# Optimization experiments

Measured on AMD Instinct MI355X. Metric: run time of the kernel, lower is better.

## Reference

```python
import jax, jax.numpy as jnp
import numpy as np

C = 512
B, W, H = 16, 64, 64
K = 128


def setup_inputs() -> dict:
    key = jax.random.key(0)
    ks = jax.random.split(key, 17)
    s = 0.02
    inp = {
        "x1": jax.random.normal(ks[0], (B, C, W, H), jnp.float32),
        "y1": jax.random.normal(ks[1], (B, K, C), jnp.float32),
        "x2": jax.random.normal(ks[2], (B, C, W, H), jnp.float32),
        "y2": jax.random.normal(ks[3], (B, K, C), jnp.float32),
        # 1x1 conv weights stored as [out, in]
        "wq1": jax.random.normal(ks[4], (C // 4, C), jnp.float32) * s,
        "bq1": jnp.zeros((C // 4,), jnp.float32),
        "wq2": jax.random.normal(ks[5], (C // 4, C), jnp.float32) * s,
        "bq2": jnp.zeros((C // 4,), jnp.float32),
        "wk1": jax.random.normal(ks[6], (C // 2, C), jnp.float32) * s,
        "bk1": jnp.zeros((C // 2,), jnp.float32),
        "wk2": jax.random.normal(ks[7], (C // 2, C), jnp.float32) * s,
        "bk2": jnp.zeros((C // 2,), jnp.float32),
        "wv1": jax.random.normal(ks[8], (C, C), jnp.float32) * s,
        "bv1": jnp.zeros((C,), jnp.float32),
        "wv2": jax.random.normal(ks[9], (C, C), jnp.float32) * s,
        "bv2": jnp.zeros((C,), jnp.float32),
        "scale": jnp.ones((1,), jnp.float32) * 0.5,  # nn.Parameter(zeros) would kill grads; nonzero for testing
    }
    return inp


def reference(x1, y1, x2, y2, wq1, bq1, wq2, bq2, wk1, bk1, wk2, bk2,
              wv1, bv1, wv2, bv2, scale):
    b, c, w, h = x1.shape
    n = w * h
    # 1x1 convs == channel-wise linear maps
    q1 = jnp.einsum('bcwh,dc->bdwh', x1, wq1) + bq1[None, :, None, None]
    q2 = jnp.einsum('bcwh,dc->bdwh', x2, wq2) + bq2[None, :, None, None]
    # concat along channels -> [B, C/2, N] -> [B, N, C/2]
    q = jnp.concatenate([q1, q2], axis=1).reshape(b, c // 2, n).transpose(0, 2, 1)
    k1 = y1 @ wk1.T + bk1  # [B, K, C/2]
    k2 = y2 @ wk2.T + bk2
    v1 = y1 @ wv1.T + bv1  # [B, K, C]
    v2 = y2 @ wv2.T + bv2
    e1 = jnp.einsum('bnd,bkd->bnk', q, k1)  # [B, N, K]
    e2 = jnp.einsum('bnd,bkd->bnk', q, k2)
    attn = jax.nn.softmax(jnp.abs(e1 - e2), axis=-1)
    # out = value^T @ attn^T : [B, C, N]
    o1 = jnp.einsum('bkc,bnk->bcn', v1, attn).reshape(b, c, w, h)
    o2 = jnp.einsum('bkc,bnk->bcn', v2, attn).reshape(b, c, w, h)
    out1 = scale[0] * o1 + x1
    out2 = scale[0] * o2 + x2
    return out1, out2
```

## Files before the change

### kernel.cpp

```cpp
#include <hip/hip_runtime.h>

typedef unsigned short u16;
typedef __attribute__((ext_vector_type(8))) short short8v;
typedef __attribute__((ext_vector_type(4))) unsigned short ushort4v;
typedef __attribute__((ext_vector_type(4))) float floatx4;

#define B_ 16
#define C_ 512
#define N_ 4096
#define K_ 128

__device__ __forceinline__ float bf2f(u16 u) {
    unsigned int x = ((unsigned int)u) << 16;
    return __builtin_bit_cast(float, x);
}
__device__ __forceinline__ u16 f2bf(float f) {
    unsigned int u = __builtin_bit_cast(unsigned int, f);
    u = u + 0x7FFFu + ((u >> 16) & 1u);
    return (u16)(u >> 16);
}
__device__ __forceinline__ void gload_lds16(const u16* g, u16* l) {
    __builtin_amdgcn_global_load_lds(
        (const __attribute__((address_space(1))) void*)g,
        (__attribute__((address_space(3))) void*)l, 16, 0, 0);
}

#define BARRIER_V8 do { \
    asm volatile("s_waitcnt vmcnt(8) lgkmcnt(0)" ::: "memory"); \
    __builtin_amdgcn_s_barrier(); \
    __builtin_amdgcn_sched_barrier(0); \
} while (0)
#define BARRIER_V0 do { \
    asm volatile("s_waitcnt vmcnt(0) lgkmcnt(0)" ::: "memory"); \
    __builtin_amdgcn_s_barrier(); \
    __builtin_amdgcn_sched_barrier(0); \
} while (0)

__global__ void conv_all(const float* __restrict__ y1, const float* __restrict__ y2,
                         const float* __restrict__ wk1, const float* __restrict__ wk2,
                         const float* __restrict__ wv1, const float* __restrict__ wv2,
                         const float* __restrict__ wq1, const float* __restrict__ wq2,
                         u16* y1b, u16* y2b, u16* wk1b, u16* wk2b, u16* wv1b, u16* wv2b,
                         u16* wq1t, u16* wq2t) {
    int tid = blockIdx.x * 256 + threadIdx.x;
    const int VBASE = 720896;
    if (tid < VBASE) {
        const float* src; u16* dst; int off;
        if (tid < 262144)      { src = y1;  dst = y1b;  off = tid; }
        else if (tid < 524288) { src = y2;  dst = y2b;  off = tid - 262144; }
        else if (tid < 557056) { src = wk1; dst = wk1b; off = tid - 524288; }
        else if (tid < 589824) { src = wk2; dst = wk2b; off = tid - 557056; }
        else if (tid < 655360) { src = wv1; dst = wv1b; off = tid - 589824; }
        else                   { src = wv2; dst = wv2b; off = tid - 655360; }
        float4 v = *(const float4*)(src + (size_t)off * 4);
        ushort4v p;
        p[0] = f2bf(v.x); p[1] = f2bf(v.y); p[2] = f2bf(v.z); p[3] = f2bf(v.w);
        *(ushort4v*)(dst + (size_t)off * 4) = p;
    } else {
        int e = tid - VBASE;
        const float* s = (e >= 65536) ? wq2 : wq1;
        u16* d = (e >= 65536) ? wq2t : wq1t;
        e &= 65535;
        int dd = e >> 9;
        int c = e & 511;
        d[c * 128 + dd] = f2bf(s[dd * 512 + c]);
    }
}

__global__ void gemm_gkgv(const u16* __restrict__ y1b, const u16* __restrict__ y2b,
// ... 78 lines not shown
        int koff = ch * 32 + (l >> 4) * 8;
        short8v a[4], wv[4];
#pragma unroll
        for (int mf = 0; mf < 4; ++mf) {
            size_t ro = (size_t)(m0 + mf*16 + (l & 15)) * 256 + koff;
            short8v s1 = *(const short8v*)(A1 + ro);
            short8v s2 = *(const short8v*)(A2 + ro);
            short8v av;
#pragma unroll
            for (int j = 0; j < 8; ++j)
                av[j] = (short)f2bf(bf2f((u16)s1[j]) - bf2f((u16)s2[j]));
            a[mf] = av;
        }
#pragma unroll
        for (int nf = 0; nf < 4; ++nf) wv[nf] = *(const short8v*)(Wt + (size_t)(n0 + nf*16 + (l & 15)) * 128 + koff);
#pragma unroll
        for (int mf = 0; mf < 4; ++mf)
#pragma unroll
            for (int nf = 0; nf < 4; ++nf)
                acc[mf][nf] = __builtin_amdgcn_mfma_f32_16x16x32_bf16(a[mf], wv[nf], acc[mf][nf], 0, 0, 0);
    }
#pragma unroll
    for (int mf = 0; mf < 4; ++mf)
#pragma unroll
        for (int nf = 0; nf < 4; ++nf)
#pragma unroll
            for (int rg = 0; rg < 4; ++rg) {
                int m = m0 + mf*16 + (l >> 4)*4 + rg;
                int n = n0 + nf*16 + (l & 15);
                outp[(size_t)m * C_ + n] = f2bf(acc[mf][nf][rg]);
            }
}

__global__ __launch_bounds__(256, 2)
void fused_attn(const float* __restrict__ x1, const float* __restrict__ x2,
                const u16* __restrict__ kkd1, const u16* __restrict__ kkd2,
                const u16* __restrict__ vt1, const u16* __restrict__ vt2,
                const float* __restrict__ ebd, const float* __restrict__ scale_p,
                float* __restrict__ out1, float* __restrict__ out2) {
    __shared__ u16 smem[32768];
    u16* xT[2]  = { smem,         smem + 8192 };
    u16* kkS[2] = { smem + 16384, smem + 24576 };
    u16* attn_s = smem + 16384;

    int id = blockIdx.x;
    int sw = ((id & 7) << 6) | (id >> 3);
    int b = sw >> 5;
    int n0 = (sw & 31) * 128;
    int t = threadIdx.x, w = t >> 6, l = t & 63;

    const float* xs[2] = { x1 + (size_t)b * C_ * N_, x2 + (size_t)b * C_ * N_ };
    const u16* kkp[2] = { kkd1 + (size_t)b * K_ * C_, kkd2 + (size_t)b * K_ * C_ };

    floatx4 ed[2][8] = {};

    float xA0[16], xA1[16], xB0[16], xB1[16];

    auto SLOADX = [&](int s, float (&v0)[16], float (&v1)[16]) {
        int h = s >> 3, c0 = (s & 7) * 64;
        const float* xp = xs[h] + (size_t)(c0 + w * 16) * N_ + n0 + 2 * l;
#pragma unroll
        for (int j = 0; j < 16; ++j) {
            float2 f = *(const float2*)(xp + (size_t)j * N_);
            v0[j] = f.x; v1[j] = f.y;
        }
    };
    auto KLDS = [&](int s, int buf) {
        int h = s >> 3, c0 = (s & 7) * 64;
        const u16* kp = kkp[h] + c0;
#pragma unroll
        for (int i = 0; i < 4; ++i) {
            int gi = i * 256 + t;
            int key = gi >> 3, gp = gi & 7;
            gload_lds16(kp + (size_t)key * 512 + (gp ^ (key & 7)) * 8,
                        &kkS[buf][(i * 256 + w * 64) * 8]);
        }
    };
    auto SWRITEX = [&](int buf, float (&v0)[16], float (&v1)[16]) {
        short8v p00, p01, p10, p11;
#pragma unroll
        for (int j = 0; j < 8; ++j) {
            p00[j] = (short)f2bf(v0[j]);  p01[j] = (short)f2bf(v0[j + 8]);
            p10[j] = (short)f2bf(v1[j]);  p11[j] = (short)f2bf(v1[j + 8]);
        }
        u16* xb = xT[buf];
        int row0 = 2 * l, sz = l & 7;
        *(short8v*)&xb[row0 * 64 + 8 * ((w * 2) ^ sz)] = p00;
        *(short8v*)&xb[row0 * 64 + 8 * ((w * 2 + 1) ^ sz)] = p01;
        *(short8v*)&xb[(row0 + 1) * 64 + 8 * ((w * 2) ^ sz)] = p10;
        *(short8v*)&xb[(row0 + 1) * 64 + 8 * ((w * 2 + 1) ^ sz)] = p11;
    };
    auto COMPUTE = [&](int buf) {
        u16* xb = xT[buf]; u16* kb = kkS[buf];
#pragma unroll
        for (int cc = 0; cc < 2; ++cc) {
            short8v a[2];
#pragma unroll
            for (int mf = 0; mf < 2; ++mf) {
                int row = w * 32 + mf * 16 + (l & 15);
                int g = cc * 4 + (l >> 4);
                a[mf] = *(const short8v*)&xb[row * 64 + 8 * (g ^ ((row >> 1) & 7))];
            }
#pragma unroll
            for (int kf = 0; kf < 8; ++kf) {
                int key = kf * 16 + (l & 15);
                int g = cc * 4 + (l >> 4);
                short8v bb = *(const short8v*)&kb[key * 64 + 8 * (g ^ (key & 7))];
#pragma unroll
                for (int mf = 0; mf < 2; ++mf)
                    ed[mf][kf] = __builtin_amdgcn_mfma_f32_16x16x32_bf16(a[mf], bb, ed[mf][kf], 0, 0, 0);
            }
        }
    };

    SLOADX(0, xA0, xA1); KLDS(0, 0);
    SWRITEX(0, xA0, xA1);
    SLOADX(1, xB0, xB1); KLDS(1, 1);
#pragma unroll
    for (int rr = 0; rr < 8; ++rr) {
        int sA = 2 * rr, sB = 2 * rr + 1;
        BARRIER_V8;
        if (rr > 0) KLDS(sB, 1);
        COMPUTE(0);
        SWRITEX(1, xB0, xB1);
        if (sA + 2 <= 15) SLOADX(sA + 2, xA0, xA1);
        if (rr == 7) { BARRIER_V0; }
        else         { BARRIER_V8; }
        if (sA + 2 <= 15) KLDS(sA + 2, 0);
        COMPUTE(1);
        if (sB + 1 <= 15) SWRITEX(0, xA0, xA1);
        if (sB + 2 <= 15) SLOADX(sB + 2, xB0, xB1);
    }

    float ebv[8];
#pragma unroll
    for (int kf = 0; kf < 8; ++kf) ebv[kf] = ebd[b * 128 + kf * 16 + (l & 15)];
#pragma unroll
    for (int mf = 0; mf < 2; ++mf)
#pragma unroll
        for (int kf = 0; kf < 8; ++kf)
#pragma unroll
            for (int rg = 0; rg < 4; ++rg)
                ed[mf][kf][rg] = fabsf(ed[mf][kf][rg] + ebv[kf]);

    float mx[2][4], sm[2][4];
#pragma unroll
    for (int mf = 0; mf < 2; ++mf)
#pragma unroll
        for (int rg = 0; rg < 4; ++rg) {
            float m = fmaxf(ed[mf][0][rg], ed[mf][1][rg]);
            m = fmaxf(m, fmaxf(ed[mf][2][rg], ed[mf][3][rg]));
            m = fmaxf(m, fmaxf(ed[mf][4][rg], ed[mf][5][rg]));
            m = fmaxf(m, fmaxf(ed[mf][6][rg], ed[mf][7][rg]));
            mx[mf][rg] = m;
        }
#pragma unroll
    for (int st = 1; st < 16; st <<= 1)
#pragma unroll
        for (int mf = 0; mf < 2; ++mf)
#pragma unroll
            for (int rg = 0; rg < 4; ++rg)
                mx[mf][rg] = fmaxf(mx[mf][rg], __shfl_xor(mx[mf][rg], st));
#pragma unroll
    for (int mf = 0; mf < 2; ++mf)
#pragma unroll
        for (int rg = 0; rg < 4; ++rg) sm[mf][rg] = 0.f;
#pragma unroll
    for (int mf = 0; mf < 2; ++mf)
#pragma unroll
        for (int kf = 0; kf < 8; ++kf)
#pragma unroll
            for (int rg = 0; rg < 4; ++rg) {
                float e = __expf(ed[mf][kf][rg] - mx[mf][rg]);
                ed[mf][kf][rg] = e;
                sm[mf][rg] += e;
            }
#pragma unroll
    for (int st = 1; st < 16; st <<= 1)
#pragma unroll
        for (int mf = 0; mf < 2; ++mf)
#pragma unroll
            for (int rg = 0; rg < 4; ++rg)
                sm[mf][rg] += __shfl_xor(sm[mf][rg], st);
#pragma unroll
    for (int mf = 0; mf < 2; ++mf)
#pragma unroll
        for (int rg = 0; rg < 4; ++rg) sm[mf][rg] = 1.0f / sm[mf][rg];

    __syncthreads();
#pragma unroll
    for (int mf = 0; mf < 2; ++mf)
#pragma unroll
        for (int rg = 0; rg < 4; ++rg) {
            int row = w * 32 + mf * 16 + (l >> 4) * 4 + rg;
#pragma unroll
            for (int kf = 0; kf < 8; ++kf) {
                int col = kf * 16 + (l & 15);
                attn_s[row * 128 + 8 * ((col >> 3) ^ (row & 15)) + (col & 7)] =
                    f2bf(ed[mf][kf][rg] * sm[mf][rg]);
            }
        }
    __syncthreads();

    const float sc = scale_p[0];
    const u16* vts[2] = { vt1 + (size_t)b * C_ * K_, vt2 + (size_t)b * C_ * K_ };
    float* outs[2] = { out1 + (size_t)b * C_ * N_, out2 + (size_t)b * C_ * N_ };

    short8v vfA[4], vfB[4];
    float rsA[4][8], rsB[4][8];
    auto LOADPV = [&](int s, short8v (&vf)[4], float (&rs)[4][8]) {
        int oi = s >> 3, cc = s & 7;
        const u16* vp = vts[oi] + (size_t)(cc * 64 + w * 16 + (l & 15)) * K_ + (l >> 4) * 8;
#pragma unroll
        for (int kc = 0; kc < 4; ++kc) vf[kc] = *(const short8v*)(vp + kc * 32);
        const float* rp = xs[oi] + (size_t)(cc * 64 + w * 16 + (l >> 4) * 4) * N_ + n0 + (l & 15);
#pragma unroll
        for (int rg = 0; rg < 4; ++rg)
#pragma unroll
            for (int nf = 0; nf < 8; ++nf)
                rs[rg][nf] = rp[(size_t)rg * N_ + nf * 16];
    };
    auto COMPPV = [&](int s, short8v (&vf)[4], float (&rs)[4][8]) {
        floatx4 o[8] = {};
#pragma unroll
        for (int kc = 0; kc < 4; ++kc) {
#pragma unroll
            for (int nf = 0; nf < 8; ++nf) {
                int row = nf * 16 + (l & 15);
                int g = kc * 4 + (l >> 4);
                short8v bb = *(const short8v*)&attn_s[row * 128 + 8 * (g ^ (row & 15))];
                o[nf] = __builtin_amdgcn_mfma_f32_16x16x32_bf16(vf[kc], bb, o[nf], 0, 0, 0);
            }
        }
        int oi = s >> 3, cc = s & 7;
        float* op = outs[oi];
        int cr = cc * 64 + w * 16 + (l >> 4) * 4;
#pragma unroll
        for (int rg = 0; rg < 4; ++rg) {
            size_t rowoff = (size_t)(cr + rg) * N_ + n0 + (l & 15);
#pragma unroll
            for (int nf = 0; nf < 8; ++nf)
                op[rowoff + nf * 16] = sc * o[nf][rg] + rs[rg][nf];
        }
    };

    LOADPV(0, vfA, rsA);
    LOADPV(1, vfB, rsB);
#pragma unroll
    for (int ss = 0; ss < 8; ++ss) {
        COMPPV(2 * ss, vfA, rsA);
        if (2 * ss + 2 < 16) LOADPV(2 * ss + 2, vfA, rsA);
        COMPPV(2 * ss + 1, vfB, rsB);
        if (2 * ss + 3 < 16) LOADPV(2 * ss + 3, vfB, rsB);
    }
}

extern "C" void kernel_launch(void* const* d_in, const int* in_sizes, int n_in,
                              void* d_out, int out_size, void* d_ws, size_t ws_size,
                              hipStream_t stream) {
    const float* x1 = (const float*)d_in[0];
    const float* y1 = (const float*)d_in[1];
    const float* x2 = (const float*)d_in[2];
    const float* y2 = (const float*)d_in[3];
    const float* wq1 = (const float*)d_in[4];
    const float* bq1 = (const float*)d_in[5];
    const float* wq2 = (const float*)d_in[6];
    const float* bq2 = (const float*)d_in[7];
    const float* wk1 = (const float*)d_in[8];
    const float* bk1 = (const float*)d_in[9];
    const float* wk2 = (const float*)d_in[10];
    const float* bk2 = (const float*)d_in[11];
    const float* wv1 = (const float*)d_in[12];
    const float* bv1 = (const float*)d_in[13];
    const float* wv2 = (const float*)d_in[14];
    const float* bv2 = (const float*)d_in[15];
    const float* scale = (const float*)d_in[16];

    char* ws = (char*)d_ws;
    u16* y1b  = (u16*)(ws + 0);
    u16* y2b  = (u16*)(ws + 2097152);
    u16* wk1b = (u16*)(ws + 4194304);
    u16* wk2b = (u16*)(ws + 4456448);
    u16* wv1b = (u16*)(ws + 4718592);
    u16* wv2b = (u16*)(ws + 5242880);
    u16* wq1t = (u16*)(ws + 5767168);
    u16* wq2t = (u16*)(ws + 5898240);
    u16* k1b  = (u16*)(ws + 6029312);
    u16* k2b  = (u16*)(ws + 7077888);
    u16* kkd1 = (u16*)(ws + 9175040);
    u16* kkd2 = (u16*)(ws + 11272192);
    u16* vt1  = (u16*)(ws + 13369344);
    u16* vt2  = (u16*)(ws + 15466496);
    float* ebd = (float*)(ws + 17563648);

    float* out1 = (float*)d_out;
    float* out2 = out1 + (size_t)B_ * C_ * N_;

    hipLaunchKernelGGL(conv_all, dim3(3328), dim3(256), 0, stream,
                       y1, y2, wk1, wk2, wv1, wv2, wq1, wq2,
                       y1b, y2b, wk1b, wk2b, wv1b, wv2b, wq1t, wq2t);
    hipLaunchKernelGGL(gemm_gkgv, dim3(768), dim3(64), 0, stream,
                       y1b, y2b, wk1b, wk2b, wv1b, wv2b, bk1, bk2, bv1, bv2,
                       k1b, k2b, vt1, vt2);
    hipLaunchKernelGGL(gemm_gkk_ebd, dim3(544), dim3(64), 0, stream,
                       k1b, k2b, wq1t, wq2t, bq1, bq2, kkd1, kkd2, ebd);
    hipLaunchKernelGGL(fused_attn, dim3(512), dim3(256), 0, stream,
                       x1, x2, kkd1, kkd2, vt1, vt2, ebd, scale, out1, out2);
}
```

Before: 213.2 us.

## Process two N-tiles per block, overlapping second QK pass with first PV pass

Each block of the fused attention kernel now handles two 128-column tiles, so the grid is halved to 256 blocks. While the PV output pass of the first tile runs, the QK score accumulation of the second tile proceeds in the same loop, interleaving MFMA work with the x/K loads. LDS grows to hold a separate attention buffer, and the softmax becomes a macro that runs once per tile. The risks are fewer blocks to fill the CUs (256 blocks of 256 threads), higher register pressure, and extra barriers in the merged loop.

After: 315.2 us. +47.8%, slower.

```diff
diff --git a/kernel.cpp b/kernel.cpp
--- a/kernel.cpp
+++ b/kernel.cpp
@@ -185,34 +185,43 @@
                 const u16* __restrict__ vt1, const u16* __restrict__ vt2,
                 const float* __restrict__ ebd, const float* __restrict__ scale_p,
                 float* __restrict__ out1, float* __restrict__ out2) {
-    __shared__ u16 smem[32768];
-    u16* xT[2]  = { smem,         smem + 8192 };
-    u16* kkS[2] = { smem + 16384, smem + 24576 };
-    u16* attn_s = smem + 16384;
+    __shared__ u16 smem[40960];
+    u16* xTb[2] = { smem, smem + 8192 };
+    u16* kkS0   = smem + 16384;
+    u16* attn_s = smem + 24576;
+    u16* attnlo = smem + 24576;
 
     int id = blockIdx.x;
-    int sw = ((id & 7) << 6) | (id >> 3);
-    int b = sw >> 5;
-    int n0 = (sw & 31) * 128;
+    int sw = ((id & 7) << 5) | (id >> 3);
+    int b  = sw >> 4;
+    int n0 = (sw & 15) * 256;
+    int n1 = n0 + 128;
     int t = threadIdx.x, w = t >> 6, l = t & 63;
 
     const float* xs[2] = { x1 + (size_t)b * C_ * N_, x2 + (size_t)b * C_ * N_ };
     const u16* kkp[2] = { kkd1 + (size_t)b * K_ * C_, kkd2 + (size_t)b * K_ * C_ };
+    const u16* vts[2] = { vt1 + (size_t)b * C_ * K_, vt2 + (size_t)b * C_ * K_ };
+    float* outs[2] = { out1 + (size_t)b * C_ * N_, out2 + (size_t)b * C_ * N_ };
+    const float sc = scale_p[0];
 
     floatx4 ed[2][8] = {};
+    float ebv[8];
+#pragma unroll
+    for (int kf = 0; kf < 8; ++kf) ebv[kf] = ebd[b * 128 + kf * 16 + (l & 15)];
 
     float xA0[16], xA1[16], xB0[16], xB1[16];
-
-    auto SLOADX = [&](int s, float (&v0)[16], float (&v1)[16]) {
+    short8v vfA[4], vfB[4];
+
+    auto SLOADX = [&](int n, int s, float (&v0)[16], float (&v1)[16]) {
         int h = s >> 3, c0 = (s & 7) * 64;
-        const float* xp = xs[h] + (size_t)(c0 + w * 16) * N_ + n0 + 2 * l;
+        const float* xp = xs[h] + (size_t)(c0 + w * 16) * N_ + n + 2 * l;
 #pragma unroll
         for (int j = 0; j < 16; ++j) {
             float2 f = *(const float2*)(xp + (size_t)j * N_);
             v0[j] = f.x; v1[j] = f.y;
         }
     };
-    auto KLDS = [&](int s, int buf) {
+    auto KLDS = [&](int s, u16* kb) {
         int h = s >> 3, c0 = (s & 7) * 64;
         const u16* kp = kkp[h] + c0;
 #pragma unroll
@@ -220,7 +229,7 @@
             int gi = i * 256 + t;
             int key = gi >> 3, gp = gi & 7;
             gload_lds16(kp + (size_t)key * 512 + (gp ^ (key & 7)) * 8,
-                        &kkS[buf][(i * 256 + w * 64) * 8]);
+                        &kb[(i * 256 + w * 64) * 8]);
         }
     };
     auto SWRITEX = [&](int buf, float (&v0)[16], float (&v1)[16]) {
@@ -230,15 +239,14 @@
             p00[j] = (short)f2bf(v0[j]);  p01[j] = (short)f2bf(v0[j + 8]);
             p10[j] = (short)f2bf(v1[j]);  p11[j] = (short)f2bf(v1[j + 8]);
         }
-        u16* xb = xT[buf];
+        u16* xb = xTb[buf];
         int row0 = 2 * l, sz = l & 7;
         *(short8v*)&xb[row0 * 64 + 8 * ((w * 2) ^ sz)] = p00;
         *(short8v*)&xb[row0 * 64 + 8 * ((w * 2 + 1) ^ sz)] = p01;
         *(short8v*)&xb[(row0 + 1) * 64 + 8 * ((w * 2) ^ sz)] = p10;
         *(short8v*)&xb[(row0 + 1) * 64 + 8 * ((w * 2 + 1) ^ sz)] = p11;
     };
-    auto COMPUTE = [&](int buf) {
-        u16* xb = xT[buf]; u16* kb = kkS[buf];
+    auto COMPUTE = [&](const u16* xb, const u16* kb) {
 #pragma unroll
         for (int cc = 0; cc < 2; ++cc) {
             short8v a[2];
@@ -259,115 +267,22 @@
             }
         }
     };
-
-    SLOADX(0, xA0, xA1); KLDS(0, 0);
-    SWRITEX(0, xA0, xA1);
-    SLOADX(1, xB0, xB1); KLDS(1, 1);
-#pragma unroll
-    for (int rr = 0; rr < 8; ++rr) {
-        int sA = 2 * rr, sB = 2 * rr + 1;
-        BARRIER_V8;
-        if (rr > 0) KLDS(sB, 1);
-        COMPUTE(0);
-        SWRITEX(1, xB0, xB1);
-        if (sA + 2 <= 15) SLOADX(sA + 2, xA0, xA1);
-        if (rr == 7) { BARRIER_V0; }
-        else         { BARRIER_V8; }
-        if (sA + 2 <= 15) KLDS(sA + 2, 0);
-        COMPUTE(1);
-        if (sB + 1 <= 15) SWRITEX(0, xA0, xA1);
-        if (sB + 2 <= 15) SLOADX(sB + 2, xB0, xB1);
-    }
-
-    float ebv[8];
-#pragma unroll
-    for (int kf = 0; kf < 8; ++kf) ebv[kf] = ebd[b * 128 + kf * 16 + (l & 15)];
-#pragma unroll
-    for (int mf = 0; mf < 2; ++mf)
-#pragma unroll
-        for (int kf = 0; kf < 8; ++kf)
-#pragma unroll
-            for (int rg = 0; rg < 4; ++rg)
-                ed[mf][kf][rg] = fabsf(ed[mf][kf][rg] + ebv[kf]);
-
-    float mx[2][4], sm[2][4];
-#pragma unroll
-    for (int mf = 0; mf < 2; ++mf)
-#pragma unroll
-        for (int rg = 0; rg < 4; ++rg) {
-            float m = fmaxf(ed[mf][0][rg], ed[mf][1][rg]);
-            m = fmaxf(m, fmaxf(ed[mf][2][rg], ed[mf][3][rg]));
-            m = fmaxf(m, fmaxf(ed[mf][4][rg], ed[mf][5][rg]));
-            m = fmaxf(m, fmaxf(ed[mf][6][rg], ed[mf][7][rg]));
-            mx[mf][rg] = m;
-        }
-#pragma unroll
-    for (int st = 1; st < 16; st <<= 1)
-#pragma unroll
-        for (int mf = 0; mf < 2; ++mf)
-#pragma unroll
-            for (int rg = 0; rg < 4; ++rg)
-                mx[mf][rg] = fmaxf(mx[mf][rg], __shfl_xor(mx[mf][rg], st));
-#pragma unroll
-    for (int mf = 0; mf < 2; ++mf)
-#pragma unroll
-        for (int rg = 0; rg < 4; ++rg) sm[mf][rg] = 0.f;
-#pragma unroll
-    for (int mf = 0; mf < 2; ++mf)
-#pragma unroll
-        for (int kf = 0; kf < 8; ++kf)
-#pragma unroll
-            for (int rg = 0; rg < 4; ++rg) {
-                float e = __expf(ed[mf][kf][rg] - mx[mf][rg]);
-                ed[mf][kf][rg] = e;
-                sm[mf][rg] += e;
-            }
-#pragma unroll
-    for (int st = 1; st < 16; st <<= 1)
-#pragma unroll
-        for (int mf = 0; mf < 2; ++mf)
-#pragma unroll
-            for (int rg = 0; rg < 4; ++rg)
-                sm[mf][rg] += __shfl_xor(sm[mf][rg], st);
-#pragma unroll
-    for (int mf = 0; mf < 2; ++mf)
-#pragma unroll
-        for (int rg = 0; rg < 4; ++rg) sm[mf][rg] = 1.0f / sm[mf][rg];
-
-    __syncthreads();
-#pragma unroll
-    for (int mf = 0; mf < 2; ++mf)
-#pragma unroll
-        for (int rg = 0; rg < 4; ++rg) {
-            int row = w * 32 + mf * 16 + (l >> 4) * 4 + rg;
-#pragma unroll
-            for (int kf = 0; kf < 8; ++kf) {
-                int col = kf * 16 + (l & 15);
-                attn_s[row * 128 + 8 * ((col >> 3) ^ (row & 15)) + (col & 7)] =
-                    f2bf(ed[mf][kf][rg] * sm[mf][rg]);
-            }
-        }
-    __syncthreads();
-
-    const float sc = scale_p[0];
-    const u16* vts[2] = { vt1 + (size_t)b * C_ * K_, vt2 + (size_t)b * C_ * K_ };
-    float* outs[2] = { out1 + (size_t)b * C_ * N_, out2 + (size_t)b * C_ * N_ };
-
-    short8v vfA[4], vfB[4];
-    float rsA[4][8], rsB[4][8];
-    auto LOADPV = [&](int s, short8v (&vf)[4], float (&rs)[4][8]) {
+    auto LOADVF = [&](int s, short8v (&vf)[4]) {
         int oi = s >> 3, cc = s & 7;
         const u16* vp = vts[oi] + (size_t)(cc * 64 + w * 16 + (l & 15)) * K_ + (l >> 4) * 8;
 #pragma unroll
         for (int kc = 0; kc < 4; ++kc) vf[kc] = *(const short8v*)(vp + kc * 32);
-        const float* rp = xs[oi] + (size_t)(cc * 64 + w * 16 + (l >> 4) * 4) * N_ + n0 + (l & 15);
+    };
+    auto COMPPV = [&](int n, int s, short8v (&vf)[4]) {
+        int oi = s >> 3, cc = s & 7;
+        int cr = cc * 64 + w * 16 + (l >> 4) * 4;
+        float rs[4][8];
+        const float* rp = xs[oi] + (size_t)cr * N_ + n + (l & 15);
 #pragma unroll
         for (int rg = 0; rg < 4; ++rg)
 #pragma unroll
             for (int nf = 0; nf < 8; ++nf)
                 rs[rg][nf] = rp[(size_t)rg * N_ + nf * 16];
-    };
-    auto COMPPV = [&](int s, short8v (&vf)[4], float (&rs)[4][8]) {
         floatx4 o[8] = {};
 #pragma unroll
         for (int kc = 0; kc < 4; ++kc) {
@@ -379,27 +294,137 @@
                 o[nf] = __builtin_amdgcn_mfma_f32_16x16x32_bf16(vf[kc], bb, o[nf], 0, 0, 0);
             }
         }
-        int oi = s >> 3, cc = s & 7;
         float* op = outs[oi];
-        int cr = cc * 64 + w * 16 + (l >> 4) * 4;
 #pragma unroll
         for (int rg = 0; rg < 4; ++rg) {
-            size_t rowoff = (size_t)(cr + rg) * N_ + n0 + (l & 15);
+            size_t rowoff = (size_t)(cr + rg) * N_ + n + (l & 15);
 #pragma unroll
             for (int nf = 0; nf < 8; ++nf)
                 op[rowoff + nf * 16] = sc * o[nf][rg] + rs[rg][nf];
         }
     };
 
-    LOADPV(0, vfA, rsA);
-    LOADPV(1, vfB, rsB);
-#pragma unroll
-    for (int ss = 0; ss < 8; ++ss) {
-        COMPPV(2 * ss, vfA, rsA);
-        if (2 * ss + 2 < 16) LOADPV(2 * ss + 2, vfA, rsA);
-        COMPPV(2 * ss + 1, vfB, rsB);
-        if (2 * ss + 3 < 16) LOADPV(2 * ss + 3, vfB, rsB);
-    }
+#define SOFTMAX_PUBLISH() do { \
+    float mx[2][4], sm[2][4]; \
+    _Pragma("unroll") \
+    for (int mf = 0; mf < 2; ++mf) \
+        _Pragma("unroll") \
+        for (int kf = 0; kf < 8; ++kf) \
+            _Pragma("unroll") \
+            for (int rg = 0; rg < 4; ++rg) \
+                ed[mf][kf][rg] = fabsf(ed[mf][kf][rg] + ebv[kf]); \
+    _Pragma("unroll") \
+    for (int mf = 0; mf < 2; ++mf) \
+        _Pragma("unroll") \
+        for (int rg = 0; rg < 4; ++rg) { \
+            float m = fmaxf(ed[mf][0][rg], ed[mf][1][rg]); \
+            m = fmaxf(m, fmaxf(ed[mf][2][rg], ed[mf][3][rg])); \
+            m = fmaxf(m, fmaxf(ed[mf][4][rg], ed[mf][5][rg])); \
+            m = fmaxf(m, fmaxf(ed[mf][6][rg], ed[mf][7][rg])); \
+            mx[mf][rg] = m; \
+        } \
+    _Pragma("unroll") \
+    for (int st = 1; st < 16; st <<= 1) \
+        _Pragma("unroll") \
+        for (int mf = 0; mf < 2; ++mf) \
+            _Pragma("unroll") \
+            for (int rg = 0; rg < 4; ++rg) \
+                mx[mf][rg] = fmaxf(mx[mf][rg], __shfl_xor(mx[mf][rg], st)); \
+    _Pragma("unroll") \
+    for (int mf = 0; mf < 2; ++mf) \
+        _Pragma("unroll") \
+        for (int rg = 0; rg < 4; ++rg) sm[mf][rg] = 0.f; \
+    _Pragma("unroll") \
+    for (int mf = 0; mf < 2; ++mf) \
+        _Pragma("unroll") \
+        for (int kf = 0; kf < 8; ++kf) \
+            _Pragma("unroll") \
+            for (int rg = 0; rg < 4; ++rg) { \
+                float e = __expf(ed[mf][kf][rg] - mx[mf][rg]); \
+                ed[mf][kf][rg] = e; \
+                sm[mf][rg] += e; \
+            } \
+    _Pragma("unroll") \
+    for (int st = 1; st < 16; st <<= 1) \
+        _Pragma("unroll") \
+        for (int mf = 0; mf < 2; ++mf) \
+            _Pragma("unroll") \
+            for (int rg = 0; rg < 4; ++rg) \
+                sm[mf][rg] += __shfl_xor(sm[mf][rg], st); \
+    _Pragma("unroll") \
+    for (int mf = 0; mf < 2; ++mf) \
+        _Pragma("unroll") \
+        for (int rg = 0; rg < 4; ++rg) sm[mf][rg] = 1.0f / sm[mf][rg]; \
+    _Pragma("unroll") \
+    for (int mf = 0; mf < 2; ++mf) \
+        _Pragma("unroll") \
+        for (int rg = 0; rg < 4; ++rg) { \
+            int row = w * 32 + mf * 16 + (l >> 4) * 4 + rg; \
+            _Pragma("unroll") \
+            for (int kf = 0; kf < 8; ++kf) { \
+                int col = kf * 16 + (l & 15); \
+                attn_s[row * 128 + 8 * ((col >> 3) ^ (row & 15)) + (col & 7)] = \
+                    f2bf(ed[mf][kf][rg] * sm[mf][rg]); \
+            } \
+        } \
+} while (0)
+
+    u16* kkE[2] = { kkS0, attnlo };
+    SLOADX(n0, 0, xA0, xA1); KLDS(0, kkE[0]);
+    SWRITEX(0, xA0, xA1);
+    SLOADX(n0, 1, xB0, xB1); KLDS(1, kkE[1]);
+#pragma unroll
+    for (int rr = 0; rr < 8; ++rr) {
+        int sA = 2 * rr, sB = 2 * rr + 1;
+        BARRIER_V8;
+        if (rr > 0) KLDS(sB, kkE[1]);
+        COMPUTE(xTb[0], kkE[0]);
+        SWRITEX(1, xB0, xB1);
+        if (sA + 2 <= 15) SLOADX(n0, sA + 2, xA0, xA1);
+        if (rr == 7) { BARRIER_V0; }
+        else         { BARRIER_V8; }
+        if (sA + 2 <= 15) KLDS(sA + 2, kkE[0]);
+        COMPUTE(xTb[1], kkE[1]);
+        if (sB + 1 <= 15) SWRITEX(0, xA0, xA1);
+        if (sB + 2 <= 15) SLOADX(n0, sB + 2, xB0, xB1);
+    }
+    __syncthreads();
+
+    SLOADX(n1, 0, xA0, xA1);
+    KLDS(0, kkS0);
+    SOFTMAX_PUBLISH();
+    SWRITEX(0, xA0, xA1);
+    LOADVF(0, vfA);
+#pragma unroll
+    for (int mf = 0; mf < 2; ++mf)
+#pragma unroll
+        for (int kf = 0; kf < 8; ++kf)
+            ed[mf][kf] = (floatx4){0.f, 0.f, 0.f, 0.f};
+    __syncthreads();
+
+#pragma unroll
+    for (int i = 0; i < 16; ++i) {
+        COMPUTE(xTb[i & 1], kkS0);
+        __syncthreads();
+        if (i < 15) {
+            KLDS(i + 1, kkS0);
+            SLOADX(n1, i + 1, xA0, xA1);
+            if ((i + 1) & 1) LOADVF(i + 1, vfB); else LOADVF(i + 1, vfA);
+        }
+        if (i & 1) COMPPV(n0, i, vfB); else COMPPV(n0, i, vfA);
+        if (i < 15) SWRITEX((i + 1) & 1, xA0, xA1);
+        __syncthreads();
+    }
+
+    SOFTMAX_PUBLISH();
+    LOADVF(0, vfA);
+    __syncthreads();
+#pragma unroll
+    for (int s = 0; s < 16; ++s) {
+        if (s < 15) { if ((s + 1) & 1) LOADVF(s + 1, vfB); else LOADVF(s + 1, vfA); }
+        if (s & 1) COMPPV(n1, s, vfB); else COMPPV(n1, s, vfA);
+    }
+#undef SOFTMAX_PUBLISH
 }
 
 extern "C" void kernel_launch(void* const* d_in, const int* in_sizes, int n_in,
@@ -451,6 +476,6 @@
                        k1b, k2b, vt1, vt2);
     hipLaunchKernelGGL(gemm_gkk_ebd, dim3(544), dim3(64), 0, stream,
                        k1b, k2b, wq1t, wq2t, bq1, bq2, kkd1, kkd2, ebd);
-    hipLaunchKernelGGL(fused_attn, dim3(512), dim3(256), 0, stream,
+    hipLaunchKernelGGL(fused_attn, dim3(256), dim3(256), 0, stream,
                        x1, x2, kkd1, kkd2, vt1, vt2, ebd, scale, out1, out2);
 }
```

## Warp-specialize fused attention so energy and PV phases overlap across tiles

Applied to the files above, without the earlier changes.

The fused attention kernel becomes a 512-thread block that handles two 128-column tiles. Four waves compute energies and softmax for one tile while the other four waves run the PV product and residual store for the previous tile. The attention buffer is double-buffered in LDS, which doubles shared memory to 128KB. The goal is to overlap the memory-heavy PV/store phase with the MFMA-heavy energy phase, at the cost of a three-stage pipeline with a drained first and last stage, fewer blocks in flight, and register/LDS pressure that may limit occupancy.

Measured after the change: 452.0 us. 112% more time.

```diff
diff --git a/kernel.cpp b/kernel.cpp
--- a/kernel.cpp
+++ b/kernel.cpp
@@ -24,17 +24,6 @@
         (const __attribute__((address_space(1))) void*)g,
         (__attribute__((address_space(3))) void*)l, 16, 0, 0);
 }
-
-#define BARRIER_V8 do { \
-    asm volatile("s_waitcnt vmcnt(8) lgkmcnt(0)" ::: "memory"); \
-    __builtin_amdgcn_s_barrier(); \
-    __builtin_amdgcn_sched_barrier(0); \
-} while (0)
-#define BARRIER_V0 do { \
-    asm volatile("s_waitcnt vmcnt(0) lgkmcnt(0)" ::: "memory"); \
-    __builtin_amdgcn_s_barrier(); \
-    __builtin_amdgcn_sched_barrier(0); \
-} while (0)
 
 __global__ void conv_all(const float* __restrict__ y1, const float* __restrict__ y2,
                          const float* __restrict__ wk1, const float* __restrict__ wk2,
@@ -179,48 +168,59 @@
             }
 }
 
-__global__ __launch_bounds__(256, 2)
+__global__ __launch_bounds__(512, 2)
 void fused_attn(const float* __restrict__ x1, const float* __restrict__ x2,
                 const u16* __restrict__ kkd1, const u16* __restrict__ kkd2,
                 const u16* __restrict__ vt1, const u16* __restrict__ vt2,
                 const float* __restrict__ ebd, const float* __restrict__ scale_p,
                 float* __restrict__ out1, float* __restrict__ out2) {
-    __shared__ u16 smem[32768];
-    u16* xT[2]  = { smem,         smem + 8192 };
-    u16* kkS[2] = { smem + 16384, smem + 24576 };
-    u16* attn_s = smem + 16384;
+    __shared__ u16 smem[65536];
+#define XT_(i)    (smem + (i) * 8192)
+#define KKS_(i)   (smem + 16384 + (i) * 8192)
+#define ATTN_(i)  (smem + 32768 + (i) * 16384)
 
     int id = blockIdx.x;
-    int sw = ((id & 7) << 6) | (id >> 3);
-    int b = sw >> 5;
-    int n0 = (sw & 31) * 128;
+    int sw = ((id & 7) << 5) | (id >> 3);
+    int b  = sw >> 4;
+    int n0 = (sw & 15) * 256;
     int t = threadIdx.x, w = t >> 6, l = t & 63;
+    bool isE = (w < 4);
+    int wp = w & 3;
+    int tE = t & 255;
 
     const float* xs[2] = { x1 + (size_t)b * C_ * N_, x2 + (size_t)b * C_ * N_ };
     const u16* kkp[2] = { kkd1 + (size_t)b * K_ * C_, kkd2 + (size_t)b * K_ * C_ };
+    const u16* vts[2] = { vt1 + (size_t)b * C_ * K_, vt2 + (size_t)b * C_ * K_ };
+    float* outs[2] = { out1 + (size_t)b * C_ * N_, out2 + (size_t)b * C_ * N_ };
+    const float sc = scale_p[0];
 
     floatx4 ed[2][8] = {};
+    float ebv[8];
+#pragma unroll
+    for (int kf = 0; kf < 8; ++kf) ebv[kf] = ebd[b * 128 + kf * 16 + (l & 15)];
 
     float xA0[16], xA1[16], xB0[16], xB1[16];
-
-    auto SLOADX = [&](int s, float (&v0)[16], float (&v1)[16]) {
+    short8v vfA[4], vfB[4];
+    float rsA[4][8], rsB[4][8];
+
+    auto SLOADX = [&](int n, int s, float (&v0)[16], float (&v1)[16]) {
         int h = s >> 3, c0 = (s & 7) * 64;
-        const float* xp = xs[h] + (size_t)(c0 + w * 16) * N_ + n0 + 2 * l;
+        const float* xp = xs[h] + (size_t)(c0 + wp * 16) * N_ + n + 2 * l;
 #pragma unroll
         for (int j = 0; j < 16; ++j) {
             float2 f = *(const float2*)(xp + (size_t)j * N_);
             v0[j] = f.x; v1[j] = f.y;
         }
     };
-    auto KLDS = [&](int s, int buf) {
+    auto KLDS = [&](int s, u16* kb) {
         int h = s >> 3, c0 = (s & 7) * 64;
         const u16* kp = kkp[h] + c0;
 #pragma unroll
         for (int i = 0; i < 4; ++i) {
-            int gi = i * 256 + t;
+            int gi = i * 256 + tE;
             int key = gi >> 3, gp = gi & 7;
             gload_lds16(kp + (size_t)key * 512 + (gp ^ (key & 7)) * 8,
-                        &kkS[buf][(i * 256 + w * 64) * 8]);
+                        &kb[(i * 256 + wp * 64) * 8]);
         }
     };
     auto SWRITEX = [&](int buf, float (&v0)[16], float (&v1)[16]) {
@@ -230,21 +230,20 @@
             p00[j] = (short)f2bf(v0[j]);  p01[j] = (short)f2bf(v0[j + 8]);
             p10[j] = (short)f2bf(v1[j]);  p11[j] = (short)f2bf(v1[j + 8]);
         }
-        u16* xb = xT[buf];
+        u16* xb = XT_(buf);
         int row0 = 2 * l, sz = l & 7;
-        *(short8v*)&xb[row0 * 64 + 8 * ((w * 2) ^ sz)] = p00;
-        *(short8v*)&xb[row0 * 64 + 8 * ((w * 2 + 1) ^ sz)] = p01;
-        *(short8v*)&xb[(row0 + 1) * 64 + 8 * ((w * 2) ^ sz)] = p10;
-        *(short8v*)&xb[(row0 + 1) * 64 + 8 * ((w * 2 + 1) ^ sz)] = p11;
-    };
-    auto COMPUTE = [&](int buf) {
-        u16* xb = xT[buf]; u16* kb = kkS[buf];
+        *(short8v*)&xb[row0 * 64 + 8 * ((wp * 2) ^ sz)] = p00;
+        *(short8v*)&xb[row0 * 64 + 8 * ((wp * 2 + 1) ^ sz)] = p01;
+        *(short8v*)&xb[(row0 + 1) * 64 + 8 * ((wp * 2) ^ sz)] = p10;
+        *(short8v*)&xb[(row0 + 1) * 64 + 8 * ((wp * 2 + 1) ^ sz)] = p11;
+    };
+    auto COMPUTE = [&](const u16* xb, const u16* kb) {
 #pragma unroll
         for (int cc = 0; cc < 2; ++cc) {
             short8v a[2];
 #pragma unroll
             for (int mf = 0; mf < 2; ++mf) {
-                int row = w * 32 + mf * 16 + (l & 15);
+                int row = wp * 32 + mf * 16 + (l & 15);
                 int g = cc * 4 + (l >> 4);
                 a[mf] = *(const short8v*)&xb[row * 64 + 8 * (g ^ ((row >> 1) & 7))];
             }
@@ -259,115 +258,19 @@
             }
         }
     };
-
-    SLOADX(0, xA0, xA1); KLDS(0, 0);
-    SWRITEX(0, xA0, xA1);
-    SLOADX(1, xB0, xB1); KLDS(1, 1);
-#pragma unroll
-    for (int rr = 0; rr < 8; ++rr) {
-        int sA = 2 * rr, sB = 2 * rr + 1;
-        BARRIER_V8;
-        if (rr > 0) KLDS(sB, 1);
-        COMPUTE(0);
-        SWRITEX(1, xB0, xB1);
-        if (sA + 2 <= 15) SLOADX(sA + 2, xA0, xA1);
-        if (rr == 7) { BARRIER_V0; }
-        else         { BARRIER_V8; }
-        if (sA + 2 <= 15) KLDS(sA + 2, 0);
-        COMPUTE(1);
-        if (sB + 1 <= 15) SWRITEX(0, xA0, xA1);
-        if (sB + 2 <= 15) SLOADX(sB + 2, xB0, xB1);
-    }
-
-    float ebv[8];
-#pragma unroll
-    for (int kf = 0; kf < 8; ++kf) ebv[kf] = ebd[b * 128 + kf * 16 + (l & 15)];
-#pragma unroll
-    for (int mf = 0; mf < 2; ++mf)
-#pragma unroll
-        for (int kf = 0; kf < 8; ++kf)
-#pragma unroll
-            for (int rg = 0; rg < 4; ++rg)
-                ed[mf][kf][rg] = fabsf(ed[mf][kf][rg] + ebv[kf]);
-
-    float mx[2][4], sm[2][4];
-#pragma unroll
-    for (int mf = 0; mf < 2; ++mf)
-#pragma unroll
-        for (int rg = 0; rg < 4; ++rg) {
-            float m = fmaxf(ed[mf][0][rg], ed[mf][1][rg]);
-            m = fmaxf(m, fmaxf(ed[mf][2][rg], ed[mf][3][rg]));
-            m = fmaxf(m, fmaxf(ed[mf][4][rg], ed[mf][5][rg]));
-            m = fmaxf(m, fmaxf(ed[mf][6][rg], ed[mf][7][rg]));
-            mx[mf][rg] = m;
-        }
-#pragma unroll
-    for (int st = 1; st < 16; st <<= 1)
-#pragma unroll
-        for (int mf = 0; mf < 2; ++mf)
-#pragma unroll
-            for (int rg = 0; rg < 4; ++rg)
-                mx[mf][rg] = fmaxf(mx[mf][rg], __shfl_xor(mx[mf][rg], st));
-#pragma unroll
-    for (int mf = 0; mf < 2; ++mf)
-#pragma unroll
-        for (int rg = 0; rg < 4; ++rg) sm[mf][rg] = 0.f;
-#pragma unroll
-    for (int mf = 0; mf < 2; ++mf)
-#pragma unroll
-        for (int kf = 0; kf < 8; ++kf)
-#pragma unroll
-            for (int rg = 0; rg < 4; ++rg) {
-                float e = __expf(ed[mf][kf][rg] - mx[mf][rg]);
-                ed[mf][kf][rg] = e;
-                sm[mf][rg] += e;
-            }
-#pragma unroll
-    for (int st = 1; st < 16; st <<= 1)
-#pragma unroll
-        for (int mf = 0; mf < 2; ++mf)
-#pragma unroll
-            for (int rg = 0; rg < 4; ++rg)
-                sm[mf][rg] += __shfl_xor(sm[mf][rg], st);
-#pragma unroll
-    for (int mf = 0; mf < 2; ++mf)
-#pragma unroll
-        for (int rg = 0; rg < 4; ++rg) sm[mf][rg] = 1.0f / sm[mf][rg];
-
-    __syncthreads();
-#pragma unroll
-    for (int mf = 0; mf < 2; ++mf)
-#pragma unroll
-        for (int rg = 0; rg < 4; ++rg) {
-            int row = w * 32 + mf * 16 + (l >> 4) * 4 + rg;
-#pragma unroll
-            for (int kf = 0; kf < 8; ++kf) {
-                int col = kf * 16 + (l & 15);
-                attn_s[row * 128 + 8 * ((col >> 3) ^ (row & 15)) + (col & 7)] =
-                    f2bf(ed[mf][kf][rg] * sm[mf][rg]);
-            }
-        }
-    __syncthreads();
-
-    const float sc = scale_p[0];
-    const u16* vts[2] = { vt1 + (size_t)b * C_ * K_, vt2 + (size_t)b * C_ * K_ };
-    float* outs[2] = { out1 + (size_t)b * C_ * N_, out2 + (size_t)b * C_ * N_ };
-
-    short8v vfA[4], vfB[4];
-    float rsA[4][8], rsB[4][8];
-    auto LOADPV = [&](int s, short8v (&vf)[4], float (&rs)[4][8]) {
+    auto LOADPV = [&](int n, int s, short8v (&vf)[4], float (&rs)[4][8]) {
         int oi = s >> 3, cc = s & 7;
-        const u16* vp = vts[oi] + (size_t)(cc * 64 + w * 16 + (l & 15)) * K_ + (l >> 4) * 8;
+        const u16* vp = vts[oi] + (size_t)(cc * 64 + wp * 16 + (l & 15)) * K_ + (l >> 4) * 8;
 #pragma unroll
         for (int kc = 0; kc < 4; ++kc) vf[kc] = *(const short8v*)(vp + kc * 32);
-        const float* rp = xs[oi] + (size_t)(cc * 64 + w * 16 + (l >> 4) * 4) * N_ + n0 + (l & 15);
+        const float* rp = xs[oi] + (size_t)(cc * 64 + wp * 16 + (l >> 4) * 4) * N_ + n + (l & 15);
 #pragma unroll
         for (int rg = 0; rg < 4; ++rg)
 #pragma unroll
             for (int nf = 0; nf < 8; ++nf)
                 rs[rg][nf] = rp[(size_t)rg * N_ + nf * 16];
     };
-    auto COMPPV = [&](int s, short8v (&vf)[4], float (&rs)[4][8]) {
+    auto COMPPV = [&](int n, int s, short8v (&vf)[4], float (&rs)[4][8], const u16* at) {
         floatx4 o[8] = {};
 #pragma unroll
         for (int kc = 0; kc < 4; ++kc) {
@@ -375,31 +278,156 @@
             for (int nf = 0; nf < 8; ++nf) {
                 int row = nf * 16 + (l & 15);
                 int g = kc * 4 + (l >> 4);
-                short8v bb = *(const short8v*)&attn_s[row * 128 + 8 * (g ^ (row & 15))];
+                short8v bb = *(const short8v*)&at[row * 128 + 8 * (g ^ (row & 15))];
                 o[nf] = __builtin_amdgcn_mfma_f32_16x16x32_bf16(vf[kc], bb, o[nf], 0, 0, 0);
             }
         }
         int oi = s >> 3, cc = s & 7;
         float* op = outs[oi];
-        int cr = cc * 64 + w * 16 + (l >> 4) * 4;
+        int cr = cc * 64 + wp * 16 + (l >> 4) * 4;
 #pragma unroll
         for (int rg = 0; rg < 4; ++rg) {
-            size_t rowoff = (size_t)(cr + rg) * N_ + n0 + (l & 15);
+            size_t rowoff = (size_t)(cr + rg) * N_ + n + (l & 15);
 #pragma unroll
             for (int nf = 0; nf < 8; ++nf)
                 op[rowoff + nf * 16] = sc * o[nf][rg] + rs[rg][nf];
         }
     };
-
-    LOADPV(0, vfA, rsA);
-    LOADPV(1, vfB, rsB);
-#pragma unroll
-    for (int ss = 0; ss < 8; ++ss) {
-        COMPPV(2 * ss, vfA, rsA);
-        if (2 * ss + 2 < 16) LOADPV(2 * ss + 2, vfA, rsA);
-        COMPPV(2 * ss + 1, vfB, rsB);
-        if (2 * ss + 3 < 16) LOADPV(2 * ss + 3, vfB, rsB);
-    }
+    auto SMPUB = [&](u16* at) {
+        float mx[2][4], sm[2][4];
+#pragma unroll
+        for (int mf = 0; mf < 2; ++mf)
+#pragma unroll
+            for (int kf = 0; kf < 8; ++kf)
+#pragma unroll
+                for (int rg = 0; rg < 4; ++rg)
+                    ed[mf][kf][rg] = fabsf(ed[mf][kf][rg] + ebv[kf]);
+#pragma unroll
+        for (int mf = 0; mf < 2; ++mf)
+#pragma unroll
+            for (int rg = 0; rg < 4; ++rg) {
+                float m = fmaxf(ed[mf][0][rg], ed[mf][1][rg]);
+                m = fmaxf(m, fmaxf(ed[mf][2][rg], ed[mf][3][rg]));
+                m = fmaxf(m, fmaxf(ed[mf][4][rg], ed[mf][5][rg]));
+                m = fmaxf(m, fmaxf(ed[mf][6][rg], ed[mf][7][rg]));
+                mx[mf][rg] = m;
+            }
+#pragma unroll
+        for (int st = 1; st < 16; st <<= 1)
+#pragma unroll
+            for (int mf = 0; mf < 2; ++mf)
+#pragma unroll
+                for (int rg = 0; rg < 4; ++rg)
+                    mx[mf][rg] = fmaxf(mx[mf][rg], __shfl_xor(mx[mf][rg], st));
+#pragma unroll
+        for (int mf = 0; mf < 2; ++mf)
+#pragma unroll
+            for (int rg = 0; rg < 4; ++rg) sm[mf][rg] = 0.f;
+#pragma unroll
+        for (int mf = 0; mf < 2; ++mf)
+#pragma unroll
+            for (int kf = 0; kf < 8; ++kf)
+#pragma unroll
+                for (int rg = 0; rg < 4; ++rg) {
+                    float e = __expf(ed[mf][kf][rg] - mx[mf][rg]);
+                    ed[mf][kf][rg] = e;
+                    sm[mf][rg] += e;
+                }
+#pragma unroll
+        for (int st = 1; st < 16; st <<= 1)
+#pragma unroll
+            for (int mf = 0; mf < 2; ++mf)
+#pragma unroll
+                for (int rg = 0; rg < 4; ++rg)
+                    sm[mf][rg] += __shfl_xor(sm[mf][rg], st);
+#pragma unroll
+        for (int mf = 0; mf < 2; ++mf)
+#pragma unroll
+            for (int rg = 0; rg < 4; ++rg) sm[mf][rg] = 1.0f / sm[mf][rg];
+#pragma unroll
+        for (int mf = 0; mf < 2; ++mf)
+#pragma unroll
+            for (int rg = 0; rg < 4; ++rg) {
+                int row = wp * 32 + mf * 16 + (l >> 4) * 4 + rg;
+#pragma unroll
+                for (int kf = 0; kf < 8; ++kf) {
+                    int col = kf * 16 + (l & 15);
+                    at[row * 128 + 8 * ((col >> 3) ^ (row & 15)) + (col & 7)] =
+                        f2bf(ed[mf][kf][rg] * sm[mf][rg]);
+                }
+            }
+    };
+
+#pragma unroll 1
+    for (int p = 0; p < 3; ++p) {
+        const bool doE = (p < 2), doPV = (p > 0);
+        const int nE = n0 + p * 128;
+        const int nPV = n0 + (p - 1) * 128;
+        u16* attn_w = ATTN_(p & 1);
+        const u16* attn_r = ATTN_((p + 1) & 1);
+
+        if (isE) {
+            if (doE) {
+                SLOADX(nE, 0, xA0, xA1); KLDS(0, KKS_(0));
+                SWRITEX(0, xA0, xA1);
+                SLOADX(nE, 1, xB0, xB1); KLDS(1, KKS_(1));
+            }
+        } else if (doPV) {
+            LOADPV(nPV, 0, vfA, rsA);
+            LOADPV(nPV, 1, vfB, rsB);
+        }
+
+#pragma unroll 1
+        for (int rr = 0; rr < 8; ++rr) {
+            int sA = 2 * rr, sB = 2 * rr + 1;
+            if (isE) asm volatile("s_waitcnt vmcnt(8) lgkmcnt(0)" ::: "memory");
+            else     asm volatile("s_waitcnt lgkmcnt(0)" ::: "memory");
+            __builtin_amdgcn_s_barrier();
+            __builtin_amdgcn_sched_barrier(0);
+            if (isE) {
+                if (doE) {
+                    if (rr > 0) KLDS(sB, KKS_(1));
+                    COMPUTE(XT_(0), KKS_(0));
+                    SWRITEX(1, xB0, xB1);
+                    if (sA + 2 <= 15) SLOADX(nE, sA + 2, xA0, xA1);
+                }
+            } else if (doPV) {
+                COMPPV(nPV, sA, vfA, rsA, attn_r);
+                if (sA + 2 <= 15) LOADPV(nPV, sA + 2, vfA, rsA);
+            }
+            if (isE) {
+                if (rr == 7) asm volatile("s_waitcnt vmcnt(0) lgkmcnt(0)" ::: "memory");
+                else         asm volatile("s_waitcnt vmcnt(8) lgkmcnt(0)" ::: "memory");
+            } else asm volatile("s_waitcnt lgkmcnt(0)" ::: "memory");
+            __builtin_amdgcn_s_barrier();
+            __builtin_amdgcn_sched_barrier(0);
+            if (isE) {
+                if (doE) {
+                    if (sA + 2 <= 15) KLDS(sA + 2, KKS_(0));
+                    COMPUTE(XT_(1), KKS_(1));
+                    if (sB + 1 <= 15) SWRITEX(0, xA0, xA1);
+                    if (sB + 2 <= 15) SLOADX(nE, sB + 2, xB0, xB1);
+                }
+            } else if (doPV) {
+                COMPPV(nPV, sB, vfB, rsB, attn_r);
+                if (sB + 2 <= 15) LOADPV(nPV, sB + 2, vfB, rsB);
+            }
+        }
+
+        __syncthreads();
+        if (isE && doE) {
+            SMPUB(attn_w);
+#pragma unroll
+            for (int mf = 0; mf < 2; ++mf)
+#pragma unroll
+                for (int kf = 0; kf < 8; ++kf)
+                    ed[mf][kf] = (floatx4){0.f, 0.f, 0.f, 0.f};
+        }
+        __syncthreads();
+    }
+#undef XT_
+#undef KKS_
+#undef ATTN_
 }
 
 extern "C" void kernel_launch(void* const* d_in, const int* in_sizes, int n_in,
@@ -451,6 +479,6 @@
                        k1b, k2b, vt1, vt2);
     hipLaunchKernelGGL(gemm_gkk_ebd, dim3(544), dim3(64), 0, stream,
                        k1b, k2b, wq1t, wq2t, bq1, bq2, kkd1, kkd2, ebd);
-    hipLaunchKernelGGL(fused_attn, dim3(512), dim3(256), 0, stream,
+    hipLaunchKernelGGL(fused_attn, dim3(256), dim3(512), 0, stream,
                        x1, x2, kkd1, kkd2, vt1, vt2, ebd, scale, out1, out2);
 }
```

## Halve QK channel stage depth and LDS footprint to raise occupancy to four blocks

Applied to the files above, without the earlier changes.

Shrinks each QK-stage channel chunk from 64 to 32, halving the x-tile and K-tile LDS buffers (64KB to 32KB) and the per-thread staging registers, and bumps launch bounds to four blocks per CU. The attention tile now aliases the x buffer region instead of the K region. It also hoists the first PV prefetch (V fragment and residual x) to before the softmax so its latency overlaps the epilogue. The trade-off is twice as many pipeline stages and barriers, plus tighter register pressure under the larger occupancy bound, which may cause spills.

Result: slower. 341.6 us (+60.2%).

```diff
diff --git a/kernel.cpp b/kernel.cpp
--- a/kernel.cpp
+++ b/kernel.cpp
@@ -179,16 +179,16 @@
             }
 }
 
-__global__ __launch_bounds__(256, 2)
+__global__ __launch_bounds__(256, 4)
 void fused_attn(const float* __restrict__ x1, const float* __restrict__ x2,
                 const u16* __restrict__ kkd1, const u16* __restrict__ kkd2,
                 const u16* __restrict__ vt1, const u16* __restrict__ vt2,
                 const float* __restrict__ ebd, const float* __restrict__ scale_p,
                 float* __restrict__ out1, float* __restrict__ out2) {
-    __shared__ u16 smem[32768];
-    u16* xT[2]  = { smem,         smem + 8192 };
-    u16* kkS[2] = { smem + 16384, smem + 24576 };
-    u16* attn_s = smem + 16384;
+    __shared__ u16 smem[16384];
+    u16* xT[2]  = { smem,        smem + 4096 };
+    u16* kkS[2] = { smem + 8192, smem + 12288 };
+    u16* attn_s = smem;
 
     int id = blockIdx.x;
     int sw = ((id & 7) << 6) | (id >> 3);
@@ -201,83 +201,95 @@
 
     floatx4 ed[2][8] = {};
 
-    float xA0[16], xA1[16], xB0[16], xB1[16];
-
-    auto SLOADX = [&](int s, float (&v0)[16], float (&v1)[16]) {
-        int h = s >> 3, c0 = (s & 7) * 64;
-        const float* xp = xs[h] + (size_t)(c0 + w * 16) * N_ + n0 + 2 * l;
-#pragma unroll
-        for (int j = 0; j < 16; ++j) {
+    float xA[16], xB[16];
+
+    auto SLOADX = [&](int s, float (&v)[16]) {
+        int h = s >> 4, c0 = (s & 15) * 32;
+        const float* xp = xs[h] + (size_t)(c0 + w * 8) * N_ + n0 + 2 * l;
+#pragma unroll
+        for (int j = 0; j < 8; ++j) {
             float2 f = *(const float2*)(xp + (size_t)j * N_);
-            v0[j] = f.x; v1[j] = f.y;
-        }
+            v[2 * j] = f.x; v[2 * j + 1] = f.y;
+        }
+    };
+    auto SWRITEX = [&](int buf, float (&v)[16]) {
+        short8v p0, p1;
+#pragma unroll
+        for (int j = 0; j < 8; ++j) { p0[j] = (short)f2bf(v[2 * j]); p1[j] = (short)f2bf(v[2 * j + 1]); }
+        u16* xb = xT[buf];
+        int row0 = 2 * l;
+        int pos = 8 * (w ^ (l & 3));
+        *(short8v*)&xb[row0 * 32 + pos] = p0;
+        *(short8v*)&xb[(row0 + 1) * 32 + pos] = p1;
     };
     auto KLDS = [&](int s, int buf) {
-        int h = s >> 3, c0 = (s & 7) * 64;
+        int h = s >> 4, c0 = (s & 15) * 32;
         const u16* kp = kkp[h] + c0;
 #pragma unroll
-        for (int i = 0; i < 4; ++i) {
+        for (int i = 0; i < 2; ++i) {
             int gi = i * 256 + t;
-            int key = gi >> 3, gp = gi & 7;
-            gload_lds16(kp + (size_t)key * 512 + (gp ^ (key & 7)) * 8,
+            int key = gi >> 2, gp = gi & 3;
+            gload_lds16(kp + (size_t)key * 512 + (gp ^ ((key >> 1) & 3)) * 8,
                         &kkS[buf][(i * 256 + w * 64) * 8]);
         }
-    };
-    auto SWRITEX = [&](int buf, float (&v0)[16], float (&v1)[16]) {
-        short8v p00, p01, p10, p11;
-#pragma unroll
-        for (int j = 0; j < 8; ++j) {
-            p00[j] = (short)f2bf(v0[j]);  p01[j] = (short)f2bf(v0[j + 8]);
-            p10[j] = (short)f2bf(v1[j]);  p11[j] = (short)f2bf(v1[j + 8]);
-        }
-        u16* xb = xT[buf];
-        int row0 = 2 * l, sz = l & 7;
-        *(short8v*)&xb[row0 * 64 + 8 * ((w * 2) ^ sz)] = p00;
-        *(short8v*)&xb[row0 * 64 + 8 * ((w * 2 + 1) ^ sz)] = p01;
-        *(short8v*)&xb[(row0 + 1) * 64 + 8 * ((w * 2) ^ sz)] = p10;
-        *(short8v*)&xb[(row0 + 1) * 64 + 8 * ((w * 2 + 1) ^ sz)] = p11;
     };
     auto COMPUTE = [&](int buf) {
         u16* xb = xT[buf]; u16* kb = kkS[buf];
-#pragma unroll
-        for (int cc = 0; cc < 2; ++cc) {
-            short8v a[2];
-#pragma unroll
-            for (int mf = 0; mf < 2; ++mf) {
-                int row = w * 32 + mf * 16 + (l & 15);
-                int g = cc * 4 + (l >> 4);
-                a[mf] = *(const short8v*)&xb[row * 64 + 8 * (g ^ ((row >> 1) & 7))];
-            }
-#pragma unroll
-            for (int kf = 0; kf < 8; ++kf) {
-                int key = kf * 16 + (l & 15);
-                int g = cc * 4 + (l >> 4);
-                short8v bb = *(const short8v*)&kb[key * 64 + 8 * (g ^ (key & 7))];
-#pragma unroll
-                for (int mf = 0; mf < 2; ++mf)
-                    ed[mf][kf] = __builtin_amdgcn_mfma_f32_16x16x32_bf16(a[mf], bb, ed[mf][kf], 0, 0, 0);
-            }
-        }
-    };
-
-    SLOADX(0, xA0, xA1); KLDS(0, 0);
-    SWRITEX(0, xA0, xA1);
-    SLOADX(1, xB0, xB1); KLDS(1, 1);
-#pragma unroll
-    for (int rr = 0; rr < 8; ++rr) {
+        int g = l >> 4;
+        short8v a[2];
+#pragma unroll
+        for (int mf = 0; mf < 2; ++mf) {
+            int row = w * 32 + mf * 16 + (l & 15);
+            a[mf] = *(const short8v*)&xb[row * 32 + 8 * (g ^ (((l & 15) >> 1) & 3))];
+        }
+#pragma unroll
+        for (int kf = 0; kf < 8; ++kf) {
+            int key = kf * 16 + (l & 15);
+            short8v bb = *(const short8v*)&kb[key * 32 + 8 * (g ^ (((l & 15) >> 1) & 3))];
+#pragma unroll
+            for (int mf = 0; mf < 2; ++mf)
+                ed[mf][kf] = __builtin_amdgcn_mfma_f32_16x16x32_bf16(a[mf], bb, ed[mf][kf], 0, 0, 0);
+        }
+    };
+
+    SLOADX(0, xA); KLDS(0, 0);
+    SWRITEX(0, xA);
+    SLOADX(1, xB); KLDS(1, 1);
+#pragma unroll
+    for (int rr = 0; rr < 16; ++rr) {
         int sA = 2 * rr, sB = 2 * rr + 1;
         BARRIER_V8;
         if (rr > 0) KLDS(sB, 1);
         COMPUTE(0);
-        SWRITEX(1, xB0, xB1);
-        if (sA + 2 <= 15) SLOADX(sA + 2, xA0, xA1);
-        if (rr == 7) { BARRIER_V0; }
-        else         { BARRIER_V8; }
-        if (sA + 2 <= 15) KLDS(sA + 2, 0);
+        SWRITEX(1, xB);
+        if (sA + 2 <= 31) SLOADX(sA + 2, xA);
+        if (rr == 15) { BARRIER_V0; }
+        else          { BARRIER_V8; }
+        if (sA + 2 <= 31) KLDS(sA + 2, 0);
         COMPUTE(1);
-        if (sB + 1 <= 15) SWRITEX(0, xA0, xA1);
-        if (sB + 2 <= 15) SLOADX(sB + 2, xB0, xB1);
-    }
+        if (sB + 1 <= 31) SWRITEX(0, xA);
+        if (sB + 2 <= 31) SLOADX(sB + 2, xB);
+    }
+
+    const float sc = scale_p[0];
+    const u16* vts[2] = { vt1 + (size_t)b * C_ * K_, vt2 + (size_t)b * C_ * K_ };
+    float* outs[2] = { out1 + (size_t)b * C_ * N_, out2 + (size_t)b * C_ * N_ };
+
+    short8v vfA[4], vfB[4];
+    float rsA[4][8], rsB[4][8];
+    auto LOADPV = [&](int s, short8v (&vf)[4], float (&rs)[4][8]) {
+        int oi = s >> 3, cc = s & 7;
+        const u16* vp = vts[oi] + (size_t)(cc * 64 + w * 16 + (l & 15)) * K_ + (l >> 4) * 8;
+#pragma unroll
+        for (int kc = 0; kc < 4; ++kc) vf[kc] = *(const short8v*)(vp + kc * 32);
+        const float* rp = xs[oi] + (size_t)(cc * 64 + w * 16 + (l >> 4) * 4) * N_ + n0 + (l & 15);
+#pragma unroll
+        for (int rg = 0; rg < 4; ++rg)
+#pragma unroll
+            for (int nf = 0; nf < 8; ++nf)
+                rs[rg][nf] = rp[(size_t)rg * N_ + nf * 16];
+    };
+    LOADPV(0, vfA, rsA);
 
     float ebv[8];
 #pragma unroll
@@ -349,24 +361,6 @@
         }
     __syncthreads();
 
-    const float sc = scale_p[0];
-    const u16* vts[2] = { vt1 + (size_t)b * C_ * K_, vt2 + (size_t)b * C_ * K_ };
-    float* outs[2] = { out1 + (size_t)b * C_ * N_, out2 + (size_t)b * C_ * N_ };
-
-    short8v vfA[4], vfB[4];
-    float rsA[4][8], rsB[4][8];
-    auto LOADPV = [&](int s, short8v (&vf)[4], float (&rs)[4][8]) {
-        int oi = s >> 3, cc = s & 7;
-        const u16* vp = vts[oi] + (size_t)(cc * 64 + w * 16 + (l & 15)) * K_ + (l >> 4) * 8;
-#pragma unroll
-        for (int kc = 0; kc < 4; ++kc) vf[kc] = *(const short8v*)(vp + kc * 32);
-        const float* rp = xs[oi] + (size_t)(cc * 64 + w * 16 + (l >> 4) * 4) * N_ + n0 + (l & 15);
-#pragma unroll
-        for (int rg = 0; rg < 4; ++rg)
-#pragma unroll
-            for (int nf = 0; nf < 8; ++nf)
-                rs[rg][nf] = rp[(size_t)rg * N_ + nf * 16];
-    };
     auto COMPPV = [&](int s, short8v (&vf)[4], float (&rs)[4][8]) {
         floatx4 o[8] = {};
 #pragma unroll
@@ -391,7 +385,6 @@
         }
     };
 
-    LOADPV(0, vfA, rsA);
     LOADPV(1, vfB, rsB);
 #pragma unroll
     for (int ss = 0; ss < 8; ++ss) {
```
